# Performance work log

Measured on AMD Instinct MI355X. Metric: run time of the kernel, lower is better.

Reference implementation:

```python
import jax, jax.numpy as jnp
import numpy as np

N_NODES = 100000
N_EDGES = 1600000
IN_DIM = 256
OUT_DIM = 128


def setup_inputs() -> dict:
    key = jax.random.key(0)
    k1, k2, k3, k4, k5 = jax.random.split(key, 5)
    x = jax.random.normal(k1, (N_NODES, IN_DIM), dtype=jnp.float32)
    W = jax.random.normal(k2, (OUT_DIM, IN_DIM), dtype=jnp.float32) * (1.0 / np.sqrt(IN_DIM))
    edge_row = jax.random.randint(k3, (N_EDGES,), 0, N_NODES, dtype=jnp.int32)
    edge_col = jax.random.randint(k4, (N_EDGES,), 0, N_NODES, dtype=jnp.int32)
    # normalized adjacency values (positive, like D^-1/2 A D^-1/2 entries)
    edge_val = jax.random.uniform(k5, (N_EDGES,), dtype=jnp.float32)
    return {"x": x, "W": W, "edge_row": edge_row, "edge_col": edge_col, "edge_val": edge_val}


def reference(x, W, edge_row, edge_col, edge_val):
    # h = x @ W.T  (Linear without bias), shape [N, out_dim]
    h = jnp.einsum('ni,oi->no', x, W)
    # SpMM: out[r] = sum_{e: row[e]==r} val[e] * h[col[e]]
    msgs = h[edge_col] * edge_val[:, None]           # [E, out_dim] irregular gather
    out = jax.ops.segment_sum(msgs, edge_row, num_segments=x.shape[0])
    return out
```

## Files before the change

kernel.cpp:

```cpp
#include <hip/hip_runtime.h>
#include <hip/hip_fp16.h>

#define N_NODES 100000
#define N_EDGES 1600000
#define IN_DIM  256
#define OUT_DIM 128

#define BROWS  256
#define NBKT   391
#define CAP    4608
#define CHUNK  8192
#define NBLK   196
#define DCAP   6144

#define BMT    32
#define NTILE  (N_NODES / BMT)
#define TPB    4
#define NGBLK  ((NTILE + TPB - 1) / TPB)
#define BUFSZ  (BMT * 512)

typedef __attribute__((ext_vector_type(8))) short short8;
typedef __attribute__((ext_vector_type(4))) float f32x4;
typedef __attribute__((ext_vector_type(2))) float f32x2;

__device__ __forceinline__ unsigned short f2bf(float f) {
    unsigned int u = __float_as_uint(f);
    u += 0x7FFFu + ((u >> 16) & 1u);
    return (unsigned short)(u >> 16);
}
__device__ __forceinline__ float bf2f(unsigned int u16) {
    return __uint_as_float(u16 << 16);
}

__device__ __forceinline__ short8 pack8(float4 a, float4 b) {
    short8 s;
    s[0] = (short)f2bf(a.x); s[1] = (short)f2bf(a.y);
    s[2] = (short)f2bf(a.z); s[3] = (short)f2bf(a.w);
    s[4] = (short)f2bf(b.x); s[5] = (short)f2bf(b.y);
    s[6] = (short)f2bf(b.z); s[7] = (short)f2bf(b.w);
    return s;
}

__global__ __launch_bounds__(256) void w_to_bf16(const float* __restrict__ W,
                                                 unsigned short* __restrict__ Wb,
                                                 int* __restrict__ bcnt) {
    int i = blockIdx.x * 256 + threadIdx.x;
    if (i < OUT_DIM * IN_DIM) Wb[i] = f2bf(W[i]);
    if (blockIdx.x == 0) {
        for (int b = threadIdx.x; b < NBKT; b += 256) bcnt[b] = 0;
    }
}

__global__ __launch_bounds__(512) void gemm_bin(const float* __restrict__ x,
                                                const unsigned short* __restrict__ Wb,
                                                unsigned short* __restrict__ hb,
                                                const int* __restrict__ erow,
                                                const int* __restrict__ ecol,
                                                const float* __restrict__ eval,
                                                int* __restrict__ bcnt,
                                                int2* __restrict__ gbuf) {
    __shared__ unsigned short xs[2 * BMT * 256];
    const int tid = threadIdx.x;

    if (blockIdx.x < NBLK) {
        int* h    = (int*)xs;
        int* gpos = h + NBKT;
        int* rcur = gpos + NBKT;
        for (int i = tid; i < NBKT; i += 512) { h[i] = 0; rcur[i] = 0; }
        __syncthreads();
        const int e0 = blockIdx.x * CHUNK;
        for (int i = tid; i < CHUNK; i += 512) {
            int e = e0 + i;
            if (e < N_EDGES) atomicAdd(&h[erow[e] >> 8], 1);
        }
        __syncthreads();
        for (int i = tid; i < NBKT; i += 512)
            gpos[i] = h[i] ? (i * CAP + atomicAdd(&bcnt[i], h[i])) : 0;
        __syncthreads();
        for (int i = tid; i < CHUNK; i += 512) {
            int e = e0 + i;
            if (e < N_EDGES) {
                int r = erow[e];
                int b = r >> 8;
                unsigned int vb  = __half_as_ushort(__float2half(eval[e]));
                unsigned int rec = (vb << 17) | (unsigned int)ecol[e];
                int pos = gpos[b] + atomicAdd(&rcur[b], 1);
                gbuf[pos] = make_int2((int)rec, r);
            }
        }
        return;
    }

    const int g    = blockIdx.x - NBLK;
    const int t0   = g * TPB;
    const int wid  = tid >> 6;
    const int lane = tid & 63;
    const int l15  = lane & 15;
    const int g8   = (lane >> 4) * 8;
    const int col  = wid * 16 + l15;
    const int sw   = (l15 & 7) << 4;
    char* lb = (char*)xs;

    const int srow = tid >> 4;
    const int ca   = (tid & 15) * 8;
    const int swr  = (srow & 7) << 4;
    const int wbA  = (srow * 512 + ca * 2) ^ swr;
    const int wbB  = (srow * 512 + (ca + 128) * 2) ^ swr;

    short8 bfr[8];
    const unsigned short* wrow = Wb + (size_t)col * IN_DIM + g8;
#pragma unroll
    for (int kk = 0; kk < 8; ++kk)
        bfr[kk] = *(const short8*)(wrow + kk * 32);

#define LDROW(ti, f0, f1, f2, f3)                                              \
    do {                                                                       \
        const int gr_ = ((ti) < NTILE) ? ((ti) * BMT + srow) : srow;           \
        const float4* sA_ = (const float4*)(x + (size_t)gr_ * IN_DIM + ca);    \
        const float4* sB_ = (const float4*)(x + (size_t)gr_ * IN_DIM + ca + 128); \
        f0 = sA_[0]; f1 = sA_[1]; f2 = sB_[0]; f3 = sB_[1];                    \
    } while (0)

    {
        float4 p0, p1, p2, p3;
        LDROW(t0, p0, p1, p2, p3);
        *(short8*)(lb + wbA) = pack8(p0, p1);
        *(short8*)(lb + wbB) = pack8(p2, p3);
    }

#pragma unroll
    for (int i = 0; i < TPB; ++i) {
        __syncthreads();

        float4 q0, q1, q2, q3;
        if (i + 1 < TPB) {
            LDROW(t0 + i + 1, q0, q1, q2, q3);
        }

        const int ti = t0 + i;
        const char* cb = lb + (i & 1) * BUFSZ;
        short8 a0[8], a1[8];
#pragma unroll
        for (int kk = 0; kk < 8; ++kk) {
            a0[kk] = *(const short8*)(cb + ((l15 * 512 + (kk * 32 + g8) * 2) ^ sw));
            a1[kk] = *(const short8*)(cb + (((l15 + 16) * 512 + (kk * 32 + g8) * 2) ^ sw));
        }
        f32x4 acc0 = {0.f, 0.f, 0.f, 0.f}, acc1 = {0.f, 0.f, 0.f, 0.f};
#pragma unroll
        for (int kk = 0; kk < 8; ++kk) {
            acc0 = __builtin_amdgcn_mfma_f32_16x16x32_bf16(a0[kk], bfr[kk], acc0, 0, 0, 0);
            acc1 = __builtin_amdgcn_mfma_f32_16x16x32_bf16(a1[kk], bfr[kk], acc1, 0, 0, 0);
        }
        if (ti < NTILE) {
            const int rb0 = ti * BMT + (lane >> 4) * 4;
            const int rb1 = rb0 + 16;
#pragma unroll
            for (int q = 0; q < 4; ++q) {
                hb[(size_t)(rb0 + q) * OUT_DIM + col] = f2bf(acc0[q]);
                hb[(size_t)(rb1 + q) * OUT_DIM + col] = f2bf(acc1[q]);
            }
        }

        if (i + 1 < TPB) {
            char* wbuf = lb + ((i + 1) & 1) * BUFSZ;
            *(short8*)(wbuf + wbA) = pack8(q0, q1);
            *(short8*)(wbuf + wbB) = pack8(q2, q3);
        }
    }
#undef LDROW
}

__global__ __launch_bounds__(512) void sort_bucket(const int2* __restrict__ gbuf,
                                                   const int* __restrict__ bcnt,
                                                   unsigned int* __restrict__ gcsr,
                                                   int* __restrict__ offs,
                                                   int* __restrict__ bend) {
    __shared__ int rh[BROWS], rc[BROWS], tmp[256];
    __shared__ unsigned int lout[DCAP];
    const int b    = blockIdx.x;
    const int base = b * CAP;
    const int cnt  = bcnt[b];
    const int r0   = b * BROWS;
    const int t    = threadIdx.x;

    if (t < BROWS) rh[t] = 0;
    __syncthreads();
    for (int i = t; i < cnt; i += 512)
        atomicAdd(&rh[gbuf[base + i].y - r0], 1);
    __syncthreads();

    int v = (t < 256) ? rh[t] : 0;
    if (t < 256) tmp[t] = v;
    __syncthreads();
    for (int d = 1; d < 256; d <<= 1) {
        int a = (t < 256 && t >= d) ? tmp[t - d] : 0;
        __syncthreads();
        if (t < 256) tmp[t] += a;
        __syncthreads();
    }
    if (t < 256) {
        int ex = tmp[t] - v;
        rc[t] = ex;
        offs[r0 + t] = base + ex;
    }
    if (t == 0) bend[b] = base + cnt;
    __syncthreads();

    if (cnt <= DCAP) {
        for (int i = t; i < cnt; i += 512) {
            int2 rr = gbuf[base + i];
            int p = atomicAdd(&rc[rr.y - r0], 1);
            lout[p] = (unsigned int)rr.x;
        }
        __syncthreads();
        for (int i = t; i < cnt; i += 512)
            gcsr[base + i] = lout[i];
    } else {
        for (int i = t; i < cnt; i += 512) {
            int2 rr = gbuf[base + i];
            int p = atomicAdd(&rc[rr.y - r0], 1);
            gcsr[base + p] = (unsigned int)rr.x;
        }
    }
}

__global__ __launch_bounds__(256) void spmm_gather(const unsigned short* __restrict__ hb,
                                                   const int* __restrict__ offs,
                                                   const int* __restrict__ bend,
                                                   const unsigned int* __restrict__ ccv,
                                                   float* __restrict__ out) {
    const int lane = threadIdx.x & 63;
    const int half = lane >> 5;
    const int li   = lane & 31;
    const int r    = blockIdx.x * 8 + (threadIdx.x >> 6) * 2 + half;

    const int js = offs[r];
    const int je = ((r & (BROWS - 1)) == (BROWS - 1)) ? bend[r >> 8] : offs[r + 1];

    f32x2 accA = {0.f, 0.f}, accB = {0.f, 0.f};
    for (int j = js; __any(j < je); j += 8) {
        unsigned int e[8];
        uint2 p[8];
#pragma unroll
        for (int q = 0; q < 8; ++q) {
            int jj = j + q;
            e[q] = ccv[jj < je ? jj : 0];
        }
#pragma unroll
        for (int q = 0; q < 8; ++q)
            p[q] = *(const uint2*)(hb + (size_t)(e[q] & 0x1FFFFu) * OUT_DIM + li * 4);
#pragma unroll
        for (int q = 0; q < 8; ++q) {
            float v = (j + q < je)
                    ? __half2float(__ushort_as_half((unsigned short)(e[q] >> 17)))
                    : 0.f;
            f32x2 vv  = {v, v};
            f32x2 h01 = { __uint_as_float(p[q].x << 16),
                          __uint_as_float(p[q].x & 0xFFFF0000u) };
            f32x2 h23 = { __uint_as_float(p[q].y << 16),
                          __uint_as_float(p[q].y & 0xFFFF0000u) };
            accA = __builtin_elementwise_fma(vv, h01, accA);
            accB = __builtin_elementwise_fma(vv, h23, accB);
        }
    }
    float4 o = {accA.x, accA.y, accB.x, accB.y};
    *(float4*)(out + (size_t)r * OUT_DIM + li * 4) = o;
}

__global__ __launch_bounds__(512) void gemm_plain(const float* __restrict__ x,
                                                  const float* __restrict__ W,
                                                  unsigned short* __restrict__ hb) {
    __shared__ unsigned short xs[2 * BMT * 256];
    const int tid = threadIdx.x;
    const int m0  = blockIdx.x * (2 * BMT);
    char* lb = (char*)xs;
    {
        const int row = tid >> 3;
        const int cs  = (tid & 7) * 32;
        const int gr  = m0 + row;
        if (gr < N_NODES) {
            const float4* src = (const float4*)(x + (size_t)gr * IN_DIM + cs);
#pragma unroll
            for (int i = 0; i < 4; ++i) {
                float4 a = src[2 * i], b = src[2 * i + 1];
                int byt = (row * 512 + (cs + 8 * i) * 2) ^ ((row & 7) << 4);
                *(short8*)(lb + byt) = pack8(a, b);
            }
        } else {
            short8 z = {0, 0, 0, 0, 0, 0, 0, 0};
#pragma unroll
            for (int i = 0; i < 4; ++i) {
                int byt = (row * 512 + (cs + 8 * i) * 2) ^ ((row & 7) << 4);
                *(short8*)(lb + byt) = z;
            }
        }
    }
    __syncthreads();
    const int wid  = tid >> 6;
    const int lane = tid & 63;
    const int l15  = lane & 15;
    const int g8   = (lane >> 4) * 8;
    short8 bfr[8];
    const float* wrowf = W + (size_t)(wid * 16 + l15) * IN_DIM + g8;
#pragma unroll
    for (int kk = 0; kk < 8; ++kk) {
        float4 wa = *(const float4*)(wrowf + kk * 32);
        float4 wb = *(const float4*)(wrowf + kk * 32 + 4);
        bfr[kk] = pack8(wa, wb);
    }
    const int col = wid * 16 + l15;
    const int sw  = (l15 & 7) << 4;
    const char* lbc = (const char*)xs;
#pragma unroll
    for (int rp = 0; rp < 2; ++rp) {
        const int r0 = rp * 32 + l15;
        const int r1 = r0 + 16;
        short8 a0[8], a1[8];
#pragma unroll
        for (int kk = 0; kk < 8; ++kk) {
            a0[kk] = *(const short8*)(lbc + ((r0 * 512 + (kk * 32 + g8) * 2) ^ sw));
            a1[kk] = *(const short8*)(lbc + ((r1 * 512 + (kk * 32 + g8) * 2) ^ sw));
        }
        f32x4 acc0 = {0.f, 0.f, 0.f, 0.f}, acc1 = {0.f, 0.f, 0.f, 0.f};
#pragma unroll
        for (int kk = 0; kk < 8; ++kk) {
            acc0 = __builtin_amdgcn_mfma_f32_16x16x32_bf16(a0[kk], bfr[kk], acc0, 0, 0, 0);
            acc1 = __builtin_amdgcn_mfma_f32_16x16x32_bf16(a1[kk], bfr[kk], acc1, 0, 0, 0);
        }
        const int rb0 = m0 + rp * 32 + (lane >> 4) * 4;
        const int rb1 = rb0 + 16;
#pragma unroll
        for (int i = 0; i < 4; ++i) {
            if (rb0 + i < N_NODES) hb[(size_t)(rb0 + i) * OUT_DIM + col] = f2bf(acc0[i]);
            if (rb1 + i < N_NODES) hb[(size_t)(rb1 + i) * OUT_DIM + col] = f2bf(acc1[i]);
        }
    }
}

__global__ __launch_bounds__(256) void spmm_scatter(const unsigned short* __restrict__ hb,
                                                    const int* __restrict__ erow,
                                                    const int* __restrict__ ecol,
                                                    const float* __restrict__ eval,
                                                    float* __restrict__ out) {
    const int lane = threadIdx.x & 63;
    const int eloc = threadIdx.x >> 6;
    const int stride = gridDim.x * 4;
    for (int e = blockIdx.x * 4 + eloc; e < N_EDGES; e += stride) {
        const int r = erow[e];
        const int c = ecol[e];
        const float v = eval[e];
        unsigned int p = *(const unsigned int*)(hb + (size_t)c * OUT_DIM + lane * 2);
        float* o = out + (size_t)r * OUT_DIM + lane * 2;
        unsafeAtomicAdd(o + 0, v * bf2f(p & 0xFFFFu));
        unsafeAtomicAdd(o + 1, v * bf2f(p >> 16));
    }
}

extern "C" void kernel_launch(void* const* d_in, const int* in_sizes, int n_in,
                              void* d_out, int out_size, void* d_ws, size_t ws_size,
                              hipStream_t stream) {
    const float* x    = (const float*)d_in[0];
    const float* W    = (const float*)d_in[1];
    const int*   erow = (const int*)d_in[2];
    const int*   ecol = (const int*)d_in[3];
    const float* eval = (const float*)d_in[4];
    float*       out  = (float*)d_out;

    const size_t H_ELEMS = (size_t)N_NODES * OUT_DIM;
    unsigned short* hb    = (unsigned short*)d_ws;
    int2*           gbuf  = (int2*)(hb + H_ELEMS);
    unsigned int*   gcsr  = (unsigned int*)(gbuf + (size_t)NBKT * CAP);
    int*            offs  = (int*)(gcsr + (size_t)NBKT * CAP);
    int*            bend  = offs + NBKT * BROWS + 8;
    int*            bcnt  = bend + NBKT;
    unsigned short* Wb    = (unsigned short*)(bcnt + NBKT + 8);
    const size_t need = ((char*)(Wb + OUT_DIM * IN_DIM)) - (char*)d_ws;

    if (ws_size >= need) {
        w_to_bf16<<<(OUT_DIM * IN_DIM + 255) / 256, 256, 0, stream>>>(W, Wb, bcnt);
        gemm_bin<<<NBLK + NGBLK, 512, 0, stream>>>(x, Wb, hb, erow, ecol, eval, bcnt, gbuf);
        sort_bucket<<<NBKT, 512, 0, stream>>>(gbuf, bcnt, gcsr, offs, bend);
        spmm_gather<<<N_NODES / 8, 256, 0, stream>>>(hb, offs, bend, gcsr, out);
    } else {
        gemm_plain<<<(N_NODES + 2 * BMT - 1) / (2 * BMT), 512, 0, stream>>>(x, W, hb);
        hipMemsetAsync(d_out, 0, (size_t)out_size * sizeof(float), stream);
        spmm_scatter<<<8192, 256, 0, stream>>>(hb, erow, ecol, eval, out);
    }
}
```

Before: 123.5 us.

## Widen SpMM gather to 16-byte loads and hoist next-tile prefetch above barrier

The SpMM gather now assigns 16 lanes per row, each loading a uint4 (eight bf16 values), so a wave covers four rows. That halves the number of gather instructions per edge and doubles the rows processed per block. In the GEMM tile loop, the global loads for the next x tile are issued before the __syncthreads instead of after it, so their latency overlaps the barrier. The trade-offs are more registers per lane and fewer lanes waiting on each row, which can make load imbalance worse for rows with many edges.

```diff
diff --git a/kernel.cpp b/kernel.cpp
--- a/kernel.cpp
+++ b/kernel.cpp
@@ -113,29 +113,27 @@
     for (int kk = 0; kk < 8; ++kk)
         bfr[kk] = *(const short8*)(wrow + kk * 32);
 
-#define LDROW(ti, f0, f1, f2, f3)                                              \
-    do {                                                                       \
-        const int gr_ = ((ti) < NTILE) ? ((ti) * BMT + srow) : srow;           \
-        const float4* sA_ = (const float4*)(x + (size_t)gr_ * IN_DIM + ca);    \
-        const float4* sB_ = (const float4*)(x + (size_t)gr_ * IN_DIM + ca + 128); \
-        f0 = sA_[0]; f1 = sA_[1]; f2 = sB_[0]; f3 = sB_[1];                    \
-    } while (0)
-
     {
-        float4 p0, p1, p2, p3;
-        LDROW(t0, p0, p1, p2, p3);
-        *(short8*)(lb + wbA) = pack8(p0, p1);
-        *(short8*)(lb + wbB) = pack8(p2, p3);
+        const int ti = t0;
+        const int gr = (ti < NTILE) ? (ti * BMT + srow) : srow;
+        const float4* sA = (const float4*)(x + (size_t)gr * IN_DIM + ca);
+        const float4* sB = (const float4*)(x + (size_t)gr * IN_DIM + ca + 128);
+        float4 f0 = sA[0], f1 = sA[1], f2 = sB[0], f3 = sB[1];
+        *(short8*)(lb + wbA) = pack8(f0, f1);
+        *(short8*)(lb + wbB) = pack8(f2, f3);
     }
 
 #pragma unroll
     for (int i = 0; i < TPB; ++i) {
-        __syncthreads();
-
         float4 q0, q1, q2, q3;
         if (i + 1 < TPB) {
-            LDROW(t0 + i + 1, q0, q1, q2, q3);
-        }
+            const int ti = t0 + i + 1;
+            const int gr = (ti < NTILE) ? (ti * BMT + srow) : srow;
+            const float4* sA = (const float4*)(x + (size_t)gr * IN_DIM + ca);
+            const float4* sB = (const float4*)(x + (size_t)gr * IN_DIM + ca + 128);
+            q0 = sA[0]; q1 = sA[1]; q2 = sB[0]; q3 = sB[1];
+        }
+        __syncthreads();
 
         const int ti = t0 + i;
         const char* cb = lb + (i & 1) * BUFSZ;
@@ -160,14 +158,12 @@
                 hb[(size_t)(rb1 + q) * OUT_DIM + col] = f2bf(acc1[q]);
             }
         }
-
         if (i + 1 < TPB) {
             char* wbuf = lb + ((i + 1) & 1) * BUFSZ;
             *(short8*)(wbuf + wbA) = pack8(q0, q1);
             *(short8*)(wbuf + wbB) = pack8(q2, q3);
         }
     }
-#undef LDROW
 }
 
 __global__ __launch_bounds__(512) void sort_bucket(const int2* __restrict__ gbuf,
@@ -230,17 +226,18 @@
                                                    const unsigned int* __restrict__ ccv,
                                                    float* __restrict__ out) {
     const int lane = threadIdx.x & 63;
-    const int half = lane >> 5;
-    const int li   = lane & 31;
-    const int r    = blockIdx.x * 8 + (threadIdx.x >> 6) * 2 + half;
+    const int qtr  = lane >> 4;
+    const int li   = lane & 15;
+    const int r    = blockIdx.x * 16 + (threadIdx.x >> 6) * 4 + qtr;
 
     const int js = offs[r];
     const int je = ((r & (BROWS - 1)) == (BROWS - 1)) ? bend[r >> 8] : offs[r + 1];
 
-    f32x2 accA = {0.f, 0.f}, accB = {0.f, 0.f};
+    f32x2 acc0 = {0.f, 0.f}, acc1 = {0.f, 0.f};
+    f32x2 acc2 = {0.f, 0.f}, acc3 = {0.f, 0.f};
     for (int j = js; __any(j < je); j += 8) {
         unsigned int e[8];
-        uint2 p[8];
+        uint4 p[8];
 #pragma unroll
         for (int q = 0; q < 8; ++q) {
             int jj = j + q;
@@ -248,23 +245,28 @@
         }
 #pragma unroll
         for (int q = 0; q < 8; ++q)
-            p[q] = *(const uint2*)(hb + (size_t)(e[q] & 0x1FFFFu) * OUT_DIM + li * 4);
+            p[q] = *(const uint4*)(hb + (size_t)(e[q] & 0x1FFFFu) * OUT_DIM + li * 8);
 #pragma unroll
         for (int q = 0; q < 8; ++q) {
             float v = (j + q < je)
                     ? __half2float(__ushort_as_half((unsigned short)(e[q] >> 17)))
                     : 0.f;
-            f32x2 vv  = {v, v};
-            f32x2 h01 = { __uint_as_float(p[q].x << 16),
-                          __uint_as_float(p[q].x & 0xFFFF0000u) };
-            f32x2 h23 = { __uint_as_float(p[q].y << 16),
-                          __uint_as_float(p[q].y & 0xFFFF0000u) };
-            accA = __builtin_elementwise_fma(vv, h01, accA);
-            accB = __builtin_elementwise_fma(vv, h23, accB);
-        }
-    }
-    float4 o = {accA.x, accA.y, accB.x, accB.y};
-    *(float4*)(out + (size_t)r * OUT_DIM + li * 4) = o;
+            f32x2 vv = {v, v};
+            f32x2 h01 = { __uint_as_float(p[q].x << 16), __uint_as_float(p[q].x & 0xFFFF0000u) };
+            f32x2 h23 = { __uint_as_float(p[q].y << 16), __uint_as_float(p[q].y & 0xFFFF0000u) };
+            f32x2 h45 = { __uint_as_float(p[q].z << 16), __uint_as_float(p[q].z & 0xFFFF0000u) };
+            f32x2 h67 = { __uint_as_float(p[q].w << 16), __uint_as_float(p[q].w & 0xFFFF0000u) };
+            acc0 = __builtin_elementwise_fma(vv, h01, acc0);
+            acc1 = __builtin_elementwise_fma(vv, h23, acc1);
+            acc2 = __builtin_elementwise_fma(vv, h45, acc2);
+            acc3 = __builtin_elementwise_fma(vv, h67, acc3);
+        }
+    }
+    float4 o0 = {acc0.x, acc0.y, acc1.x, acc1.y};
+    float4 o1 = {acc2.x, acc2.y, acc3.x, acc3.y};
+    float* dst = out + (size_t)r * OUT_DIM + li * 8;
+    *(float4*)dst       = o0;
+    *(float4*)(dst + 4) = o1;
 }
 
 __global__ __launch_bounds__(512) void gemm_plain(const float* __restrict__ x,
@@ -380,7 +382,7 @@
         w_to_bf16<<<(OUT_DIM * IN_DIM + 255) / 256, 256, 0, stream>>>(W, Wb, bcnt);
         gemm_bin<<<NBLK + NGBLK, 512, 0, stream>>>(x, Wb, hb, erow, ecol, eval, bcnt, gbuf);
         sort_bucket<<<NBKT, 512, 0, stream>>>(gbuf, bcnt, gcsr, offs, bend);
-        spmm_gather<<<N_NODES / 8, 256, 0, stream>>>(hb, offs, bend, gcsr, out);
+        spmm_gather<<<N_NODES / 16, 256, 0, stream>>>(hb, offs, bend, gcsr, out);
     } else {
         gemm_plain<<<(N_NODES + 2 * BMT - 1) / (2 * BMT), 512, 0, stream>>>(x, W, hb);
         hipMemsetAsync(d_out, 0, (size_t)out_size * sizeof(float), stream);
```

Measured after the change: 114.9 us. 7.0% less time.
